# Optimization experiments

Measured on AMD Instinct MI355X. Metric: run time of the kernel, lower is better.

## Reference

```python
import jax, jax.numpy as jnp
import numpy as np

N_NODES = 50000
N_EDGES = 1600000
IN_CH, HID_CH, OUT_CH = 384, 128, 64


def gcn_conv(x, W, b, src, dst, num_nodes):
    """PyG GCNConv: add self-loops, symmetric deg^-1/2 normalization,
    linear transform, scatter-add aggregation, bias."""
    loop = jnp.arange(num_nodes, dtype=src.dtype)
    src2 = jnp.concatenate([src, loop])  # [E+N]
    dst2 = jnp.concatenate([dst, loop])
    deg = jax.ops.segment_sum(jnp.ones_like(dst2, dtype=x.dtype), dst2,
                              num_segments=num_nodes)
    dinv = jnp.where(deg > 0, jax.lax.rsqrt(deg), 0.0)
    norm = dinv[src2] * dinv[dst2]  # [E+N]
    h = x @ W  # [N, out]
    msg = h[src2] * norm[:, None]  # gather + scale
    out = jax.ops.segment_sum(msg, dst2, num_segments=num_nodes)
    return out + b


def setup_inputs() -> dict:
    key = jax.random.key(0)
    k1, k2, k3, k4 = jax.random.split(key, 4)
    x = jax.random.normal(k1, (N_NODES, IN_CH), dtype=jnp.float32)
    edge_index = jax.random.randint(k2, (2, N_EDGES), 0, N_NODES, dtype=jnp.int64)
    W1 = jax.random.normal(k3, (IN_CH, HID_CH), dtype=jnp.float32) / np.sqrt(IN_CH)
    b1 = jnp.zeros((HID_CH,), dtype=jnp.float32)
    W2 = jax.random.normal(k4, (HID_CH, OUT_CH), dtype=jnp.float32) / np.sqrt(HID_CH)
    b2 = jnp.zeros((OUT_CH,), dtype=jnp.float32)
    return {"x": x, "edge_index": edge_index, "W1": W1, "b1": b1, "W2": W2, "b2": b2}


def reference(x, edge_index, W1, b1, W2, b2):
    src, dst = edge_index[0], edge_index[1]
    h = gcn_conv(x, W1, b1, src, dst, N_NODES)
    h = jax.nn.relu(h)
    out = gcn_conv(h, W2, b2, src, dst, N_NODES)
    return out
```

## Files before the change

### kernel.cpp

```cpp
#include <hip/hip_runtime.h>

constexpr int NN  = 50000;
constexpr int NE  = 1600000;
constexpr int CIN = 384;
constexpr int CH  = 128;
constexpr int CO  = 64;

constexpr int NB = (NN + 255) / 256;
constexpr int BUCKET_CAP = 16384;
constexpr int SCAT_EPB     = 4096;
constexpr int SCAT_BLOCKS  = (NE + SCAT_EPB - 1) / SCAT_EPB;
constexpr int G1_TILES     = (NN + 127) / 128;
constexpr int G2_TILES     = (NN + 127) / 128;

typedef __attribute__((ext_vector_type(8))) short short8;
typedef __attribute__((ext_vector_type(4))) float f32x4;


__device__ inline unsigned short f2bf(float f) {
    union { float f; unsigned int u; } v; v.f = f;
    unsigned int u = v.u + 0x7FFFu + ((v.u >> 16) & 1u);
    return (unsigned short)(u >> 16);
}
__device__ inline float bf2f(unsigned short h) { return __uint_as_float((unsigned int)h << 16); }
__device__ inline float bflo(unsigned int u) { return __uint_as_float(u << 16); }
__device__ inline float bfhi(unsigned int u) { return __uint_as_float(u & 0xFFFF0000u); }


__global__ __launch_bounds__(256) void wprep(const float* __restrict__ W1, const float* __restrict__ W2,
                                             unsigned short* __restrict__ W1t_hi, unsigned short* __restrict__ W1t_lo,
                                             unsigned short* __restrict__ W2t_hi, unsigned short* __restrict__ W2t_lo,
                                             int* __restrict__ bucket_cursor) {
    int i = blockIdx.x * 256 + threadIdx.x;
    if (blockIdx.x == 0 && threadIdx.x < NB)
        bucket_cursor[threadIdx.x] = threadIdx.x * BUCKET_CAP;
    if (i < CIN * CH) {
        int k = i / CH, c = i % CH;
        float v = W1[i];
        unsigned short h = f2bf(v);
        W1t_hi[c * CIN + k] = h;
        W1t_lo[c * CIN + k] = f2bf(v - bf2f(h));
    } else if (i < CIN * CH + CH * CO) {
        int j = i - CIN * CH;
        int k = j / CO, c = j % CO;
        float v = W2[j];
        unsigned short h = f2bf(v);
        W2t_hi[c * CH + k] = h;
        W2t_lo[c * CH + k] = f2bf(v - bf2f(h));
    }
}


__global__ __launch_bounds__(256) void fused_gemm1_scatter(const int* __restrict__ src,
                                                           const int* __restrict__ dst,
                                                           int* __restrict__ bucket_cursor,
                                                           unsigned int* __restrict__ pairs,
                                                           const float* __restrict__ X,
                                                           const unsigned short* __restrict__ Wt_hi,
                                                           const unsigned short* __restrict__ Wt_lo,
                                                           unsigned short* __restrict__ Hb) {
    __shared__ unsigned short xs_hi[128][40];
    __shared__ unsigned short xs_lo[128][40];
    __shared__ unsigned short ws_hi[128][40];
    __shared__ unsigned short ws_lo[128][40];
    __shared__ int hist[NB];
    __shared__ int base_s[NB];

    int tid = threadIdx.x;
    if (blockIdx.x < SCAT_BLOCKS) {
        int e0 = blockIdx.x * SCAT_EPB;
        for (int i = tid; i < NB; i += 256) hist[i] = 0;
        __syncthreads();
        int key[16];
        unsigned int pay[16];
        #pragma unroll
        for (int k = 0; k < 16; ++k) {
            int e = e0 + k * 256 + tid;
            if (e < NE) {
                int s = src[e], d = dst[e];
                int b = d >> 8;
                int pos = atomicAdd(&hist[b], 1);
                key[k] = b | (pos << 8);
                pay[k] = (unsigned int)s | ((unsigned int)(d & 255) << 16);
            } else {
                key[k] = -1;
            }
        }
        __syncthreads();
        for (int i = tid; i < NB; i += 256)
            base_s[i] = hist[i] ? atomicAdd(&bucket_cursor[i], hist[i]) : 0;
        __syncthreads();
        #pragma unroll
        for (int k = 0; k < 16; ++k) {
            if (key[k] >= 0) {
                int b = key[k] & 255, pos = key[k] >> 8;
                pairs[base_s[b] + pos] = pay[k];
            }
        }
        return;
    }

    int wid = tid >> 6, lane = tid & 63;
    int row0 = (blockIdx.x - SCAT_BLOCKS) * 128;
    f32x4 acc[2][8] = {};

    int xrow = tid >> 1, xc = (tid & 1) * 16;
    int grow = row0 + xrow;
    int wcol = tid >> 2, wko = (tid & 3) * 8;

    float xf[16];
    short8 pwh0, pwl0, pwh1, pwl1;

    auto loadX = [&](int k0) {
        if (grow < NN) {
            const float4* p = reinterpret_cast<const float4*>(X + (size_t)grow * CIN + k0 + xc);
            float4 v0 = p[0], v1 = p[1], v2 = p[2], v3 = p[3];
            xf[0]=v0.x; xf[1]=v0.y; xf[2]=v0.z; xf[3]=v0.w;
            xf[4]=v1.x; xf[5]=v1.y; xf[6]=v1.z; xf[7]=v1.w;
            xf[8]=v2.x; xf[9]=v2.y; xf[10]=v2.z; xf[11]=v2.w;
            xf[12]=v3.x; xf[13]=v3.y; xf[14]=v3.z; xf[15]=v3.w;
        } else {
            #pragma unroll
            for (int i = 0; i < 16; ++i) xf[i] = 0.f;
        }
    };
    auto loadW = [&](int k0) {
        pwh0 = *reinterpret_cast<const short8*>(Wt_hi + (size_t)wcol * CIN + k0 + wko);
        pwl0 = *reinterpret_cast<const short8*>(Wt_lo + (size_t)wcol * CIN + k0 + wko);
        pwh1 = *reinterpret_cast<const short8*>(Wt_hi + (size_t)(wcol + 64) * CIN + k0 + wko);
        pwl1 = *reinterpret_cast<const short8*>(Wt_lo + (size_t)(wcol + 64) * CIN + k0 + wko);
    };

    loadX(0); loadW(0);
    for (int k0 = 0; k0 < CIN; k0 += 32) {
        {
            short8 vh0, vh1, vl0, vl1;
            #pragma unroll
            for (int i = 0; i < 8; ++i) {
                unsigned short h = f2bf(xf[i]);
                vh0[i] = (short)h; vl0[i] = (short)f2bf(xf[i] - bf2f(h));
            }
            #pragma unroll
            for (int i = 0; i < 8; ++i) {
                unsigned short h = f2bf(xf[8 + i]);
                vh1[i] = (short)h; vl1[i] = (short)f2bf(xf[8 + i] - bf2f(h));
            }
            *reinterpret_cast<short8*>(&xs_hi[xrow][xc])     = vh0;
            *reinterpret_cast<short8*>(&xs_hi[xrow][xc + 8]) = vh1;
            *reinterpret_cast<short8*>(&xs_lo[xrow][xc])     = vl0;
            *reinterpret_cast<short8*>(&xs_lo[xrow][xc + 8]) = vl1;
            *reinterpret_cast<short8*>(&ws_hi[wcol][wko])      = pwh0;
            *reinterpret_cast<short8*>(&ws_lo[wcol][wko])      = pwl0;
            *reinterpret_cast<short8*>(&ws_hi[wcol + 64][wko]) = pwh1;
            *reinterpret_cast<short8*>(&ws_lo[wcol + 64][wko]) = pwl1;
        }
        __syncthreads();
        if (k0 + 32 < CIN) { loadX(k0 + 32); loadW(k0 + 32); }
        int r = lane & 15, ko = (lane >> 4) * 8;
        short8 a_hi[2], a_lo[2];
        #pragma unroll
        for (int rt = 0; rt < 2; ++rt) {
            a_hi[rt] = *reinterpret_cast<const short8*>(&xs_hi[wid * 32 + rt * 16 + r][ko]);
            a_lo[rt] = *reinterpret_cast<const short8*>(&xs_lo[wid * 32 + rt * 16 + r][ko]);
        }
        #pragma unroll
        for (int ct = 0; ct < 8; ++ct) {
            short8 b_hi = *reinterpret_cast<const short8*>(&ws_hi[ct * 16 + r][ko]);
            short8 b_lo = *reinterpret_cast<const short8*>(&ws_lo[ct * 16 + r][ko]);
            #pragma unroll
            for (int rt = 0; rt < 2; ++rt) {
                acc[rt][ct] = __builtin_amdgcn_mfma_f32_16x16x32_bf16(a_hi[rt], b_hi, acc[rt][ct], 0, 0, 0);
                acc[rt][ct] = __builtin_amdgcn_mfma_f32_16x16x32_bf16(a_hi[rt], b_lo, acc[rt][ct], 0, 0, 0);
                acc[rt][ct] = __builtin_amdgcn_mfma_f32_16x16x32_bf16(a_lo[rt], b_hi, acc[rt][ct], 0, 0, 0);
            }
        }
        __syncthreads();
    }
    int cl = lane & 15, rg = lane >> 4;
    #pragma unroll
    for (int rt = 0; rt < 2; ++rt) {
        #pragma unroll
        for (int j = 0; j < 4; ++j) {
            int row = row0 + wid * 32 + rt * 16 + rg * 4 + j;
            if (row < NN) {
                unsigned short* hp = Hb + (size_t)row * CH + cl;
                #pragma unroll
                for (int ct = 0; ct < 8; ++ct)
                    hp[ct * 16] = f2bf(acc[rt][ct][j]);
            }
        }
    }
}


__global__ __launch_bounds__(256) void bucket_scan(const int* __restrict__ bucket_cursor,
                                                   int* __restrict__ bucket_start) {
    __shared__ int tmp[256];
    int t = threadIdx.x;
    int v = (t < NB) ? (bucket_cursor[t] - t * BUCKET_CAP) : 0;
    tmp[t] = v;
    __syncthreads();
    for (int off = 1; off < 256; off <<= 1) {
        int add = (t >= off) ? tmp[t - off] : 0;
        __syncthreads();
        tmp[t] += add;
        __syncthreads();
    }
    if (t < NB) bucket_start[t] = tmp[t] - v;
    if (t == NB - 1) bucket_start[NB] = tmp[t];
}


__global__ __launch_bounds__(1024) void bucket_sort(const unsigned int* __restrict__ pairs,
                                                    const int* __restrict__ bucket_cursor,
                                                    const int* __restrict__ bucket_start,
                                                    int* __restrict__ row_start,
                                                    float* __restrict__ dinv,
                                                    unsigned short* __restrict__ csr_src) {
    __shared__ int cnt[256];
    __shared__ int pref[256];
    __shared__ int cur[256];
    int b = blockIdx.x, t = threadIdx.x;
    int p0 = b * BUCKET_CAP;
    int ne = bucket_cursor[b] - p0;
    int out0 = bucket_start[b];
    if (t < 256) cnt[t] = 0;
    __syncthreads();
    for (int i = t; i < ne; i += 1024)
        atomicAdd(&cnt[(pairs[p0 + i] >> 16) & 255], 1);
    __syncthreads();
    if (t < 256) pref[t] = cnt[t];
    __syncthreads();
    for (int off = 1; off < 256; off <<= 1) {
        int add = (t < 256 && t >= off) ? pref[t - off] : 0;
        __syncthreads();
        if (t < 256) pref[t] += add;
        __syncthreads();
    }
    if (t < 256) {
        int n = (b << 8) + t;
        if (n < NN) {
            int rs = out0 + pref[t] - cnt[t];
            row_start[n] = rs;
            cur[t] = rs;
            dinv[n] = rsqrtf((float)(cnt[t] + 1));
        }
    }
    if (b == NB - 1 && t == 0) row_start[NN] = NE;
    __syncthreads();
    for (int i = t; i < ne; i += 1024) {
        unsigned int p = pairs[p0 + i];
        int pos = atomicAdd(&cur[(p >> 16) & 255], 1);
        csr_src[pos] = (unsigned short)(p & 0xFFFF);
    }
}


__global__ __launch_bounds__(256) void gemm2_kernel(const float* __restrict__ X,
                                                    const unsigned short* __restrict__ Wt_hi,
                                                    const unsigned short* __restrict__ Wt_lo,
                                                    unsigned short* __restrict__ Hb) {
    __shared__ unsigned short xs_hi[128][40];
    __shared__ unsigned short xs_lo[128][40];
    __shared__ unsigned short ws_hi[64][40];
    __shared__ unsigned short ws_lo[64][40];

    int tid = threadIdx.x;
    int wid = tid >> 6, lane = tid & 63;
    int row0 = blockIdx.x * 128;
    f32x4 acc[2][4] = {};

    for (int k0 = 0; k0 < CH; k0 += 32) {
        {
            int row = tid >> 1, c = (tid & 1) * 16;
            int grow = row0 + row;
            float f[16];
            if (grow < NN) {
                const float4* p = reinterpret_cast<const float4*>(X + (size_t)grow * CH + k0 + c);
                float4 v0 = p[0], v1 = p[1], v2 = p[2], v3 = p[3];
                f[0]=v0.x; f[1]=v0.y; f[2]=v0.z; f[3]=v0.w;
                f[4]=v1.x; f[5]=v1.y; f[6]=v1.z; f[7]=v1.w;
                f[8]=v2.x; f[9]=v2.y; f[10]=v2.z; f[11]=v2.w;
                f[12]=v3.x; f[13]=v3.y; f[14]=v3.z; f[15]=v3.w;
            } else {
                #pragma unroll
                for (int i = 0; i < 16; ++i) f[i] = 0.f;
            }
            short8 vh0, vh1, vl0, vl1;
            #pragma unroll
            for (int i = 0; i < 8; ++i) {
                unsigned short h = f2bf(f[i]);
                vh0[i] = (short)h; vl0[i] = (short)f2bf(f[i] - bf2f(h));
            }
            #pragma unroll
            for (int i = 0; i < 8; ++i) {
                unsigned short h = f2bf(f[8 + i]);
                vh1[i] = (short)h; vl1[i] = (short)f2bf(f[8 + i] - bf2f(h));
            }
            *reinterpret_cast<short8*>(&xs_hi[row][c])     = vh0;
            *reinterpret_cast<short8*>(&xs_hi[row][c + 8]) = vh1;
            *reinterpret_cast<short8*>(&xs_lo[row][c])     = vl0;
            *reinterpret_cast<short8*>(&xs_lo[row][c + 8]) = vl1;
        }
        if (tid < 256) {
            int col = tid >> 2, ko = (tid & 3) * 8;
            *reinterpret_cast<short8*>(&ws_hi[col][ko]) =
                *reinterpret_cast<const short8*>(Wt_hi + (size_t)col * CH + k0 + ko);
            *reinterpret_cast<short8*>(&ws_lo[col][ko]) =
                *reinterpret_cast<const short8*>(Wt_lo + (size_t)col * CH + k0 + ko);
        }
        __syncthreads();
        int r = lane & 15, ko = (lane >> 4) * 8;
        short8 a_hi[2], a_lo[2];
        #pragma unroll
        for (int rt = 0; rt < 2; ++rt) {
            a_hi[rt] = *reinterpret_cast<const short8*>(&xs_hi[wid * 32 + rt * 16 + r][ko]);
            a_lo[rt] = *reinterpret_cast<const short8*>(&xs_lo[wid * 32 + rt * 16 + r][ko]);
        }
        #pragma unroll
        for (int ct = 0; ct < 4; ++ct) {
            short8 b_hi = *reinterpret_cast<const short8*>(&ws_hi[ct * 16 + r][ko]);
            short8 b_lo = *reinterpret_cast<const short8*>(&ws_lo[ct * 16 + r][ko]);
            #pragma unroll
            for (int rt = 0; rt < 2; ++rt) {
                acc[rt][ct] = __builtin_amdgcn_mfma_f32_16x16x32_bf16(a_hi[rt], b_hi, acc[rt][ct], 0, 0, 0);
                acc[rt][ct] = __builtin_amdgcn_mfma_f32_16x16x32_bf16(a_hi[rt], b_lo, acc[rt][ct], 0, 0, 0);
                acc[rt][ct] = __builtin_amdgcn_mfma_f32_16x16x32_bf16(a_lo[rt], b_hi, acc[rt][ct], 0, 0, 0);
            }
        }
        __syncthreads();
    }
    int cl = lane & 15, rg = lane >> 4;
    #pragma unroll
    for (int rt = 0; rt < 2; ++rt) {
        #pragma unroll
        for (int j = 0; j < 4; ++j) {
            int row = row0 + wid * 32 + rt * 16 + rg * 4 + j;
            if (row < NN) {
                unsigned short* hp = Hb + (size_t)row * CO + cl;
                #pragma unroll
                for (int ct = 0; ct < 4; ++ct)
                    hp[ct * 16] = f2bf(acc[rt][ct][j]);
            }
        }
    }
}


__global__ __launch_bounds__(64) void agg1_kernel(const unsigned int* __restrict__ H,
                                                  const int* __restrict__ row_start,
                                                  const unsigned short* __restrict__ csr_src,
                                                  const float* __restrict__ dinv,
                                                  const float* __restrict__ bias,
                                                  float* __restrict__ OUT) {
    int n = blockIdx.x;
    int l = threadIdx.x;
    float dn = dinv[n];
    unsigned int us = H[n * 64 + l];
    float a0 = dn * bflo(us), a1 = dn * bfhi(us);
    float b0 = 0.f, b1 = 0.f, c0 = 0.f, c1 = 0.f, d0 = 0.f, d1 = 0.f;
    int e0 = row_start[n], e1 = row_start[n + 1];
    for (int base = e0; base < e1; base += 64) {
        int m = min(64, e1 - base);
        int sv = csr_src[base + min(l, m - 1)];
        float wv = (l < m) ? dinv[sv] : 0.f;
        int j = 0;
        for (; j + 4 <= m; j += 4) {
            int s0 = __shfl(sv, j),     s1 = __shfl(sv, j + 1);
            int s2 = __shfl(sv, j + 2), s3 = __shfl(sv, j + 3);
            float w0 = __shfl(wv, j),     w1 = __shfl(wv, j + 1);
            float w2 = __shfl(wv, j + 2), w3 = __shfl(wv, j + 3);
            unsigned int u0 = H[s0 * 64 + l];
            unsigned int u1 = H[s1 * 64 + l];
            unsigned int u2 = H[s2 * 64 + l];
            unsigned int u3 = H[s3 * 64 + l];
            a0 = fmaf(w0, bflo(u0), a0); a1 = fmaf(w0, bfhi(u0), a1);
            b0 = fmaf(w1, bflo(u1), b0); b1 = fmaf(w1, bfhi(u1), b1);
            c0 = fmaf(w2, bflo(u2), c0); c1 = fmaf(w2, bfhi(u2), c1);
            d0 = fmaf(w3, bflo(u3), d0); d1 = fmaf(w3, bfhi(u3), d1);
        }
        for (; j < m; ++j) {
            int s0 = __shfl(sv, j);
            float w0 = __shfl(wv, j);
            unsigned int u0 = H[s0 * 64 + l];
            a0 = fmaf(w0, bflo(u0), a0); a1 = fmaf(w0, bfhi(u0), a1);
        }
    }
    float o0 = fmaf(dn, (a0 + b0) + (c0 + d0), reinterpret_cast<const float2*>(bias)[l].x);
    float o1 = fmaf(dn, (a1 + b1) + (c1 + d1), reinterpret_cast<const float2*>(bias)[l].y);
    reinterpret_cast<float2*>(OUT)[n * 64 + l] = make_float2(fmaxf(o0, 0.f), fmaxf(o1, 0.f));
}

__global__ __launch_bounds__(64) void agg2_kernel(const unsigned int* __restrict__ H,
                                                  const int* __restrict__ row_start,
                                                  const unsigned short* __restrict__ csr_src,
                                                  const float* __restrict__ dinv,
                                                  const float* __restrict__ bias,
                                                  float* __restrict__ OUT) {
    int n = blockIdx.x;
    int l = threadIdx.x;
    int half = l >> 5;
    int c = l & 31;
    float dn = dinv[n];
    unsigned int us = H[n * 32 + c];
    float a0 = half ? 0.f : dn * bflo(us);
    float a1 = half ? 0.f : dn * bfhi(us);
    float b0 = 0.f, b1 = 0.f;
    int e0 = row_start[n], e1 = row_start[n + 1];
    for (int base = e0; base < e1; base += 64) {
        int m = min(64, e1 - base);
        int sv = csr_src[base + min(l, m - 1)];
        float wv = (l < m) ? dinv[sv] : 0.f;
        int j = 0;
        for (; j + 4 <= m; j += 4) {
            int jj0 = j + half, jj1 = j + 2 + half;
            int s0 = __shfl(sv, jj0), s1 = __shfl(sv, jj1);
            float w0 = __shfl(wv, jj0), w1 = __shfl(wv, jj1);
            unsigned int u0 = H[s0 * 32 + c];
            unsigned int u1 = H[s1 * 32 + c];
            a0 = fmaf(w0, bflo(u0), a0); a1 = fmaf(w0, bfhi(u0), a1);
            b0 = fmaf(w1, bflo(u1), b0); b1 = fmaf(w1, bfhi(u1), b1);
        }
        for (; j < m; j += 2) {
            int jj = j + half;
            int s = __shfl(sv, min(jj, m - 1));
            float w = __shfl(wv, jj);
            unsigned int u = H[s * 32 + c];
            a0 = fmaf(w, bflo(u), a0);
            a1 = fmaf(w, bfhi(u), a1);
        }
    }
    a0 += b0; a1 += b1;
    a0 += __shfl_xor(a0, 32);
    a1 += __shfl_xor(a1, 32);
    if (l < 32) {
        float2 bv = reinterpret_cast<const float2*>(bias)[c];
        float o0 = fmaf(dn, a0, bv.x);
        float o1 = fmaf(dn, a1, bv.y);
        reinterpret_cast<float2*>(OUT)[n * 32 + c] = make_float2(o0, o1);
    }
}


extern "C" void kernel_launch(void* const* d_in, const int* in_sizes, int n_in,
                              void* d_out, int out_size, void* d_ws, size_t ws_size,
                              hipStream_t stream) {
    const float* x  = (const float*)d_in[0];
    const int*   ei = (const int*)d_in[1];
    const float* W1 = (const float*)d_in[2];
    const float* b1 = (const float*)d_in[3];
    const float* W2 = (const float*)d_in[4];
    const float* b2 = (const float*)d_in[5];
    const int* srcI = ei;
    const int* dstI = ei + NE;
    float* out = (float*)d_out;

    char* ws = (char*)d_ws;
    size_t off = 0;
    auto take = [&](size_t bytes) {
        char* p = ws + off;
        off = (off + bytes + 255) & ~(size_t)255;
        return p;
    };
    int*            row_start     = (int*)take((size_t)(NN + 1) * 4);
    int*            bucket_cursor = (int*)take((size_t)NB * 4);
    int*            bucket_start  = (int*)take((size_t)(NB + 1) * 4);
    float*          dinv          = (float*)take((size_t)NN * 4);
    unsigned short* W1t_hi        = (unsigned short*)take((size_t)CH * CIN * 2);
    unsigned short* W1t_lo        = (unsigned short*)take((size_t)CH * CIN * 2);
    unsigned short* W2t_hi        = (unsigned short*)take((size_t)CO * CH * 2);
    unsigned short* W2t_lo        = (unsigned short*)take((size_t)CO * CH * 2);
    unsigned short* csr_src       = (unsigned short*)take((size_t)NE * 2);
    unsigned short* h1b           = (unsigned short*)take((size_t)NN * CH * 2);
    float*          g1            = (float*)take((size_t)NN * CH * 4);
    unsigned short* h2b           = (unsigned short*)take((size_t)NN * CO * 2);
    unsigned int*   pairs         = (unsigned int*)g1;

    wprep<<<(CIN * CH + CH * CO + 255) / 256, 256, 0, stream>>>(W1, W2, W1t_hi, W1t_lo,
                                                                W2t_hi, W2t_lo, bucket_cursor);
    fused_gemm1_scatter<<<SCAT_BLOCKS + G1_TILES, 256, 0, stream>>>(srcI, dstI, bucket_cursor,
                                                                    pairs, x, W1t_hi, W1t_lo, h1b);
    bucket_scan<<<1, 256, 0, stream>>>(bucket_cursor, bucket_start);
    bucket_sort<<<NB, 1024, 0, stream>>>(pairs, bucket_cursor, bucket_start,
                                         row_start, dinv, csr_src);

    agg1_kernel<<<NN, 64, 0, stream>>>((const unsigned int*)h1b, row_start, csr_src, dinv, b1, g1);
    gemm2_kernel<<<G2_TILES, 256, 0, stream>>>(g1, W2t_hi, W2t_lo, h2b);
    agg2_kernel<<<NN, 64, 0, stream>>>((const unsigned int*)h2b, row_start, csr_src, dinv, b2, out);
}
```

Before: 158.2 us.

## Load MFMA operands directly from global memory, dropping LDS staging in both GEMMs

Both GEMM kernels stop staging X and W tiles through shared memory. Each lane now loads its own A fragment straight from global memory, converts it to bf16 hi/lo registers, and reads its W fragments directly from the pre-transposed global weights, so the per-iteration __syncthreads barriers go away. Launch bounds are raised to request 4 blocks per SM for higher occupancy. The trade-off is uncoalesced strided global reads and repeated W reads per wave, which are expected to be served from cache, and the software prefetch of the next k-tile in gemm1 is lost.

```diff
diff --git a/kernel.cpp b/kernel.cpp
--- a/kernel.cpp
+++ b/kernel.cpp
@@ -25,6 +25,15 @@
 __device__ inline float bf2f(unsigned short h) { return __uint_as_float((unsigned int)h << 16); }
 __device__ inline float bflo(unsigned int u) { return __uint_as_float(u << 16); }
 __device__ inline float bfhi(unsigned int u) { return __uint_as_float(u & 0xFFFF0000u); }
+
+__device__ inline void cvt8(const float* f, short8& vh, short8& vl) {
+    #pragma unroll
+    for (int i = 0; i < 8; ++i) {
+        unsigned short h = f2bf(f[i]);
+        vh[i] = (short)h;
+        vl[i] = (short)f2bf(f[i] - bf2f(h));
+    }
+}
 
 
 __global__ __launch_bounds__(256) void wprep(const float* __restrict__ W1, const float* __restrict__ W2,
@@ -51,18 +60,14 @@
 }
 
 
-__global__ __launch_bounds__(256) void fused_gemm1_scatter(const int* __restrict__ src,
-                                                           const int* __restrict__ dst,
-                                                           int* __restrict__ bucket_cursor,
-                                                           unsigned int* __restrict__ pairs,
-                                                           const float* __restrict__ X,
-                                                           const unsigned short* __restrict__ Wt_hi,
-                                                           const unsigned short* __restrict__ Wt_lo,
-                                                           unsigned short* __restrict__ Hb) {
-    __shared__ unsigned short xs_hi[128][40];
-    __shared__ unsigned short xs_lo[128][40];
-    __shared__ unsigned short ws_hi[128][40];
-    __shared__ unsigned short ws_lo[128][40];
+__global__ __launch_bounds__(256, 4) void fused_gemm1_scatter(const int* __restrict__ src,
+                                                              const int* __restrict__ dst,
+                                                              int* __restrict__ bucket_cursor,
+                                                              unsigned int* __restrict__ pairs,
+                                                              const float* __restrict__ X,
+                                                              const unsigned short* __restrict__ Wt_hi,
+                                                              const unsigned short* __restrict__ Wt_lo,
+                                                              unsigned short* __restrict__ Hb) {
     __shared__ int hist[NB];
     __shared__ int base_s[NB];
 
@@ -102,71 +107,46 @@
 
     int wid = tid >> 6, lane = tid & 63;
     int row0 = (blockIdx.x - SCAT_BLOCKS) * 128;
+    int r = lane & 15, ko = (lane >> 4) * 8;
     f32x4 acc[2][8] = {};
 
-    int xrow = tid >> 1, xc = (tid & 1) * 16;
-    int grow = row0 + xrow;
-    int wcol = tid >> 2, wko = (tid & 3) * 8;
-
-    float xf[16];
-    short8 pwh0, pwl0, pwh1, pwl1;
-
-    auto loadX = [&](int k0) {
-        if (grow < NN) {
-            const float4* p = reinterpret_cast<const float4*>(X + (size_t)grow * CIN + k0 + xc);
-            float4 v0 = p[0], v1 = p[1], v2 = p[2], v3 = p[3];
-            xf[0]=v0.x; xf[1]=v0.y; xf[2]=v0.z; xf[3]=v0.w;
-            xf[4]=v1.x; xf[5]=v1.y; xf[6]=v1.z; xf[7]=v1.w;
-            xf[8]=v2.x; xf[9]=v2.y; xf[10]=v2.z; xf[11]=v2.w;
-            xf[12]=v3.x; xf[13]=v3.y; xf[14]=v3.z; xf[15]=v3.w;
-        } else {
-            #pragma unroll
-            for (int i = 0; i < 16; ++i) xf[i] = 0.f;
-        }
-    };
-    auto loadW = [&](int k0) {
-        pwh0 = *reinterpret_cast<const short8*>(Wt_hi + (size_t)wcol * CIN + k0 + wko);
-        pwl0 = *reinterpret_cast<const short8*>(Wt_lo + (size_t)wcol * CIN + k0 + wko);
-        pwh1 = *reinterpret_cast<const short8*>(Wt_hi + (size_t)(wcol + 64) * CIN + k0 + wko);
-        pwl1 = *reinterpret_cast<const short8*>(Wt_lo + (size_t)(wcol + 64) * CIN + k0 + wko);
-    };
-
-    loadX(0); loadW(0);
+    int grow0 = row0 + wid * 32 + r;
+    int grow1 = grow0 + 16;
+    const float* xp0 = X + (size_t)grow0 * CIN + ko;
+    const float* xp1 = X + (size_t)grow1 * CIN + ko;
+    bool ok0 = grow0 < NN, ok1 = grow1 < NN;
+
     for (int k0 = 0; k0 < CIN; k0 += 32) {
+        short8 a_hi[2], a_lo[2];
         {
-            short8 vh0, vh1, vl0, vl1;
-            #pragma unroll
-            for (int i = 0; i < 8; ++i) {
-                unsigned short h = f2bf(xf[i]);
-                vh0[i] = (short)h; vl0[i] = (short)f2bf(xf[i] - bf2f(h));
-            }
-            #pragma unroll
-            for (int i = 0; i < 8; ++i) {
-                unsigned short h = f2bf(xf[8 + i]);
-                vh1[i] = (short)h; vl1[i] = (short)f2bf(xf[8 + i] - bf2f(h));
-            }
-            *reinterpret_cast<short8*>(&xs_hi[xrow][xc])     = vh0;
-            *reinterpret_cast<short8*>(&xs_hi[xrow][xc + 8]) = vh1;
-            *reinterpret_cast<short8*>(&xs_lo[xrow][xc])     = vl0;
-            *reinterpret_cast<short8*>(&xs_lo[xrow][xc + 8]) = vl1;
-            *reinterpret_cast<short8*>(&ws_hi[wcol][wko])      = pwh0;
-            *reinterpret_cast<short8*>(&ws_lo[wcol][wko])      = pwl0;
-            *reinterpret_cast<short8*>(&ws_hi[wcol + 64][wko]) = pwh1;
-            *reinterpret_cast<short8*>(&ws_lo[wcol + 64][wko]) = pwl1;
-        }
-        __syncthreads();
-        if (k0 + 32 < CIN) { loadX(k0 + 32); loadW(k0 + 32); }
-        int r = lane & 15, ko = (lane >> 4) * 8;
-        short8 a_hi[2], a_lo[2];
-        #pragma unroll
-        for (int rt = 0; rt < 2; ++rt) {
-            a_hi[rt] = *reinterpret_cast<const short8*>(&xs_hi[wid * 32 + rt * 16 + r][ko]);
-            a_lo[rt] = *reinterpret_cast<const short8*>(&xs_lo[wid * 32 + rt * 16 + r][ko]);
-        }
-        #pragma unroll
+            float f[8];
+            if (ok0) {
+                const float4* p = reinterpret_cast<const float4*>(xp0 + k0);
+                float4 v0 = p[0], v1 = p[1];
+                f[0]=v0.x; f[1]=v0.y; f[2]=v0.z; f[3]=v0.w;
+                f[4]=v1.x; f[5]=v1.y; f[6]=v1.z; f[7]=v1.w;
+            } else {
+                #pragma unroll
+                for (int i = 0; i < 8; ++i) f[i] = 0.f;
+            }
+            cvt8(f, a_hi[0], a_lo[0]);
+            if (ok1) {
+                const float4* p = reinterpret_cast<const float4*>(xp1 + k0);
+                float4 v0 = p[0], v1 = p[1];
+                f[0]=v0.x; f[1]=v0.y; f[2]=v0.z; f[3]=v0.w;
+                f[4]=v1.x; f[5]=v1.y; f[6]=v1.z; f[7]=v1.w;
+            } else {
+                #pragma unroll
+                for (int i = 0; i < 8; ++i) f[i] = 0.f;
+            }
+            cvt8(f, a_hi[1], a_lo[1]);
+        }
+        const unsigned short* wh = Wt_hi + (size_t)r * CIN + k0 + ko;
+        const unsigned short* wl = Wt_lo + (size_t)r * CIN + k0 + ko;
+        #pragma unroll 4
         for (int ct = 0; ct < 8; ++ct) {
-            short8 b_hi = *reinterpret_cast<const short8*>(&ws_hi[ct * 16 + r][ko]);
-            short8 b_lo = *reinterpret_cast<const short8*>(&ws_lo[ct * 16 + r][ko]);
+            short8 b_hi = *reinterpret_cast<const short8*>(wh + (size_t)ct * 16 * CIN);
+            short8 b_lo = *reinterpret_cast<const short8*>(wl + (size_t)ct * 16 * CIN);
             #pragma unroll
             for (int rt = 0; rt < 2; ++rt) {
                 acc[rt][ct] = __builtin_amdgcn_mfma_f32_16x16x32_bf16(a_hi[rt], b_hi, acc[rt][ct], 0, 0, 0);
@@ -174,7 +154,6 @@
                 acc[rt][ct] = __builtin_amdgcn_mfma_f32_16x16x32_bf16(a_lo[rt], b_hi, acc[rt][ct], 0, 0, 0);
             }
         }
-        __syncthreads();
     }
     int cl = lane & 15, rg = lane >> 4;
     #pragma unroll
@@ -256,71 +235,53 @@
 }
 
 
-__global__ __launch_bounds__(256) void gemm2_kernel(const float* __restrict__ X,
-                                                    const unsigned short* __restrict__ Wt_hi,
-                                                    const unsigned short* __restrict__ Wt_lo,
-                                                    unsigned short* __restrict__ Hb) {
-    __shared__ unsigned short xs_hi[128][40];
-    __shared__ unsigned short xs_lo[128][40];
-    __shared__ unsigned short ws_hi[64][40];
-    __shared__ unsigned short ws_lo[64][40];
-
+__global__ __launch_bounds__(256, 4) void gemm2_kernel(const float* __restrict__ X,
+                                                       const unsigned short* __restrict__ Wt_hi,
+                                                       const unsigned short* __restrict__ Wt_lo,
+                                                       unsigned short* __restrict__ Hb) {
     int tid = threadIdx.x;
     int wid = tid >> 6, lane = tid & 63;
     int row0 = blockIdx.x * 128;
+    int r = lane & 15, ko = (lane >> 4) * 8;
     f32x4 acc[2][4] = {};
 
+    int grow0 = row0 + wid * 32 + r;
+    int grow1 = grow0 + 16;
+    const float* xp0 = X + (size_t)grow0 * CH + ko;
+    const float* xp1 = X + (size_t)grow1 * CH + ko;
+    bool ok0 = grow0 < NN, ok1 = grow1 < NN;
+
     for (int k0 = 0; k0 < CH; k0 += 32) {
+        short8 a_hi[2], a_lo[2];
         {
-            int row = tid >> 1, c = (tid & 1) * 16;
-            int grow = row0 + row;
-            float f[16];
-            if (grow < NN) {
-                const float4* p = reinterpret_cast<const float4*>(X + (size_t)grow * CH + k0 + c);
-                float4 v0 = p[0], v1 = p[1], v2 = p[2], v3 = p[3];
+            float f[8];
+            if (ok0) {
+                const float4* p = reinterpret_cast<const float4*>(xp0 + k0);
+                float4 v0 = p[0], v1 = p[1];
                 f[0]=v0.x; f[1]=v0.y; f[2]=v0.z; f[3]=v0.w;
                 f[4]=v1.x; f[5]=v1.y; f[6]=v1.z; f[7]=v1.w;
-                f[8]=v2.x; f[9]=v2.y; f[10]=v2.z; f[11]=v2.w;
-                f[12]=v3.x; f[13]=v3.y; f[14]=v3.z; f[15]=v3.w;
             } else {
                 #pragma unroll
-                for (int i = 0; i < 16; ++i) f[i] = 0.f;
-            }
-            short8 vh0, vh1, vl0, vl1;
-            #pragma unroll
-            for (int i = 0; i < 8; ++i) {
-                unsigned short h = f2bf(f[i]);
-                vh0[i] = (short)h; vl0[i] = (short)f2bf(f[i] - bf2f(h));
-            }
-            #pragma unroll
-            for (int i = 0; i < 8; ++i) {
-                unsigned short h = f2bf(f[8 + i]);
-                vh1[i] = (short)h; vl1[i] = (short)f2bf(f[8 + i] - bf2f(h));
-            }
-            *reinterpret_cast<short8*>(&xs_hi[row][c])     = vh0;
-            *reinterpret_cast<short8*>(&xs_hi[row][c + 8]) = vh1;
-            *reinterpret_cast<short8*>(&xs_lo[row][c])     = vl0;
-            *reinterpret_cast<short8*>(&xs_lo[row][c + 8]) = vl1;
-        }
-        if (tid < 256) {
-            int col = tid >> 2, ko = (tid & 3) * 8;
-            *reinterpret_cast<short8*>(&ws_hi[col][ko]) =
-                *reinterpret_cast<const short8*>(Wt_hi + (size_t)col * CH + k0 + ko);
-            *reinterpret_cast<short8*>(&ws_lo[col][ko]) =
-                *reinterpret_cast<const short8*>(Wt_lo + (size_t)col * CH + k0 + ko);
-        }
-        __syncthreads();
-        int r = lane & 15, ko = (lane >> 4) * 8;
-        short8 a_hi[2], a_lo[2];
-        #pragma unroll
-        for (int rt = 0; rt < 2; ++rt) {
-            a_hi[rt] = *reinterpret_cast<const short8*>(&xs_hi[wid * 32 + rt * 16 + r][ko]);
-            a_lo[rt] = *reinterpret_cast<const short8*>(&xs_lo[wid * 32 + rt * 16 + r][ko]);
-        }
+                for (int i = 0; i < 8; ++i) f[i] = 0.f;
+            }
+            cvt8(f, a_hi[0], a_lo[0]);
+            if (ok1) {
+                const float4* p = reinterpret_cast<const float4*>(xp1 + k0);
+                float4 v0 = p[0], v1 = p[1];
+                f[0]=v0.x; f[1]=v0.y; f[2]=v0.z; f[3]=v0.w;
+                f[4]=v1.x; f[5]=v1.y; f[6]=v1.z; f[7]=v1.w;
+            } else {
+                #pragma unroll
+                for (int i = 0; i < 8; ++i) f[i] = 0.f;
+            }
+            cvt8(f, a_hi[1], a_lo[1]);
+        }
+        const unsigned short* wh = Wt_hi + (size_t)r * CH + k0 + ko;
+        const unsigned short* wl = Wt_lo + (size_t)r * CH + k0 + ko;
         #pragma unroll
         for (int ct = 0; ct < 4; ++ct) {
-            short8 b_hi = *reinterpret_cast<const short8*>(&ws_hi[ct * 16 + r][ko]);
-            short8 b_lo = *reinterpret_cast<const short8*>(&ws_lo[ct * 16 + r][ko]);
+            short8 b_hi = *reinterpret_cast<const short8*>(wh + (size_t)ct * 16 * CH);
+            short8 b_lo = *reinterpret_cast<const short8*>(wl + (size_t)ct * 16 * CH);
             #pragma unroll
             for (int rt = 0; rt < 2; ++rt) {
                 acc[rt][ct] = __builtin_amdgcn_mfma_f32_16x16x32_bf16(a_hi[rt], b_hi, acc[rt][ct], 0, 0, 0);
@@ -328,7 +289,6 @@
                 acc[rt][ct] = __builtin_amdgcn_mfma_f32_16x16x32_bf16(a_lo[rt], b_hi, acc[rt][ct], 0, 0, 0);
             }
         }
-        __syncthreads();
     }
     int cl = lane & 15, rg = lane >> 4;
     #pragma unroll
```

After: 270.0 us. +70.7%, slower.
